# Kernel optimization log

Hardware: AMD Instinct MI355X
Metric: run time of the kernel (lower is better)

## Reference

```python
import jax, jax.numpy as jnp
import numpy as np

EMB = 512
HEADS = 8
HEAD_DIM = EMB // HEADS


def setup_inputs() -> dict:
    key = jax.random.key(0)
    ks = jax.random.split(key, 8)
    S, B = 2048, 2
    q = jax.random.normal(ks[0], (S, B, EMB), dtype=jnp.float32)
    k = jax.random.normal(ks[1], (S, B, EMB), dtype=jnp.float32)
    v = jax.random.normal(ks[2], (S, B, EMB), dtype=jnp.float32)
    sc = 1.0 / np.sqrt(HEAD_DIM)
    Wq = jax.random.normal(ks[3], (HEAD_DIM, HEAD_DIM), dtype=jnp.float32) * sc
    Wk = jax.random.normal(ks[4], (HEAD_DIM, HEAD_DIM), dtype=jnp.float32) * sc
    Wv = jax.random.normal(ks[5], (HEAD_DIM, HEAD_DIM), dtype=jnp.float32) * sc
    Wfc = jax.random.normal(ks[6], (EMB, EMB), dtype=jnp.float32) * (1.0 / np.sqrt(EMB))
    bfc = jax.random.normal(ks[7], (EMB,), dtype=jnp.float32) * 0.01
    return {"q": q, "k": k, "v": v, "Wq": Wq, "Wk": Wk, "Wv": Wv, "Wfc": Wfc, "bfc": bfc}


def reference(q, k, v, Wq, Wk, Wv, Wfc, bfc):
    query_len, batch, emb = q.shape
    key_len = k.shape[0]
    value_len = v.shape[0]
    # Faithful to the original: plain reshape (NOT transpose) from [S,B,E] -> [B,H,S,D]
    qh = q.reshape(batch, HEADS, query_len, HEAD_DIM)
    kh = k.reshape(batch, HEADS, key_len, HEAD_DIM)
    vh = v.reshape(batch, HEADS, value_len, HEAD_DIM)
    # torch Linear(head_dim, head_dim, bias=False): y = x @ W.T
    Q = qh @ Wq.T
    K = kh @ Wk.T
    V = vh @ Wv.T
    QK = jnp.einsum('bhqd,bhkd->bhqk', Q, K)  # [B,H,S,S] score matrix (memory-bound)
    filt = jax.nn.softmax(QK / np.sqrt(HEAD_DIM).astype(np.float32), axis=3)
    att = jnp.einsum('bhqk,bhkd->bhqd', filt, V)
    att = att.reshape(query_len, batch, emb)
    return att @ Wfc.T + bfc
```

## Files before the change

### kernel.cpp

```cpp
#include <hip/hip_runtime.h>
#include <hip/hip_bf16.h>


typedef __attribute__((ext_vector_type(8))) __bf16 bf16x8;
typedef __attribute__((ext_vector_type(4))) float f32x4;
typedef __attribute__((ext_vector_type(16))) float f32x16;
typedef __attribute__((ext_vector_type(4))) unsigned short u16x4;
typedef __attribute__((ext_vector_type(4))) unsigned int u32x4;
typedef __attribute__((ext_vector_type(2))) int i32x2;
typedef unsigned short u16;
typedef unsigned int u32;

static __device__ __forceinline__ u16 f2bf(float x) {
    u32 u = __float_as_uint(x);
    u += 0x7fff + ((u >> 16) & 1);
    return (u16)(u >> 16);
}
static __device__ __forceinline__ float bf2f(u16 h) {
    return __uint_as_float(((u32)h) << 16);
}
static __device__ __forceinline__ u32 pk2(float lo, float hi) {
    __hip_bfloat162 h2 = __float22bfloat162_rn(make_float2(lo, hi));
    u32 r; __builtin_memcpy(&r, &h2, 4); return r;
}
static __device__ __forceinline__ u32 cvtpk(float lo, float hi) {
    u32 r;
    asm("v_cvt_pk_bf16_f32 %0, %1, %2" : "=v"(r) : "v"(lo), "v"(hi));
    return r;
}
static __device__ __forceinline__ void halfswap(u32 &x, u32 &y) {
#if __has_builtin(__builtin_amdgcn_permlane32_swap)
    i32x2 r = __builtin_amdgcn_permlane32_swap((int)x, (int)y, false, false);
    x = (u32)r[0]; y = (u32)r[1];
#else
    int h = (threadIdx.x >> 5) & 1;
    u32 px = (u32)__shfl_xor((int)x, 32);
    u32 py = (u32)__shfl_xor((int)y, 32);
    u32 nx = h ? py : x;
    u32 ny = h ? y : px;
    x = nx; y = ny;
#endif
}
static __device__ __forceinline__ bf16x8 mk8(u32 w0, u32 w1, u32 w2, u32 w3) {
    u32x4 u = {w0, w1, w2, w3};
    bf16x8 r; __builtin_memcpy(&r, &u, 16); return r;
}

__global__ __launch_bounds__(256) void proj_kernel(
    const float* __restrict__ q, const float* __restrict__ k, const float* __restrict__ v,
    const float* __restrict__ Wq, const float* __restrict__ Wk, const float* __restrict__ Wv,
    const float* __restrict__ Wfc,
    u16* __restrict__ Qf, u16* __restrict__ Kf, u16* __restrict__ Vf,
    u16* __restrict__ Wb, float* __restrict__ KnSq)
{
    const int mode = blockIdx.z;
    const int t = threadIdx.x;

    if (mode == 3) {
        int i = (blockIdx.x * 256 + t) * 4;
        float4 val = *(const float4*)(Wfc + i);
        uint2 b = { pk2(val.x, val.y), pk2(val.z, val.w) };
        *(uint2*)(Wb + i) = b;
        return;
    }

    const float* A = (mode == 0) ? q : (mode == 1) ? k : v;
    const float* W = (mode == 0) ? Wq : (mode == 1) ? Wk : Wv;
    const float osc = (mode == 0) ? 0.18033688011112042f : 1.0f;

    __shared__ alignas(16) u16 Ash[128 * 88];
    __shared__ alignas(16) u16 Wsh[64 * 88];
    __shared__ float red[2];

    const int m0 = blockIdx.x * 128;
    const int w = t >> 6, l = t & 63;
    const int r16 = l & 15, q4 = l >> 4;

    {
        const float4* A4 = (const float4*)(A + (size_t)m0 * 64);
        const int c4 = t & 15;
        #pragma unroll
        for (int i = 0; i < 8; ++i) {
            int row = (t >> 4) + i * 16;
            float4 val = A4[row * 16 + c4];
            uint2 bb = { pk2(val.x, val.y), pk2(val.z, val.w) };
            *(uint2*)(Ash + row * 88 + c4 * 4) = bb;
        }
        const float4* W4 = (const float4*)W;
        #pragma unroll
        for (int i = 0; i < 4; ++i) {
            int row = (t >> 4) + i * 16;
            float4 val = W4[row * 16 + c4];
            uint2 bb = { pk2(val.x, val.y), pk2(val.z, val.w) };
            *(uint2*)(Wsh + row * 88 + c4 * 4) = bb;
        }
    }
    __syncthreads();

    bf16x8 af[2][2], wf[4][2];
    #pragma unroll
    for (int mc = 0; mc < 2; ++mc)
        #pragma unroll
        for (int kk = 0; kk < 2; ++kk)
            af[mc][kk] = *(const bf16x8*)(Ash + (w * 32 + mc * 16 + r16) * 88 + kk * 32 + q4 * 8);
    #pragma unroll
    for (int nc = 0; nc < 4; ++nc)
        #pragma unroll
        for (int kk = 0; kk < 2; ++kk)
            wf[nc][kk] = *(const bf16x8*)(Wsh + (nc * 16 + r16) * 88 + kk * 32 + q4 * 8);

    f32x4 acc[2][4];
    const f32x4 zero = {0.f, 0.f, 0.f, 0.f};
    #pragma unroll
    for (int mc = 0; mc < 2; ++mc)
        #pragma unroll
        for (int nc = 0; nc < 4; ++nc) {
            acc[mc][nc] = __builtin_amdgcn_mfma_f32_16x16x32_bf16(af[mc][0], wf[nc][0], zero, 0, 0, 0);
            acc[mc][nc] = __builtin_amdgcn_mfma_f32_16x16x32_bf16(af[mc][1], wf[nc][1], acc[mc][nc], 0, 0, 0);
        }

    __syncthreads();

    const int g = m0 >> 11, t0 = (m0 & 2047) >> 6;

    if (mode < 2) {
        #pragma unroll
        for (int mc = 0; mc < 2; ++mc)
            #pragma unroll
            for (int nc = 0; nc < 4; ++nc)
                #pragma unroll
                for (int r = 0; r < 4; ++r)
                    Ash[(w * 32 + mc * 16 + q4 * 4 + r) * 72 + nc * 16 + r16] = f2bf(acc[mc][nc][r] * osc);
        __syncthreads();
        u16* Out = (mode == 0) ? Qf : Kf;
        #pragma unroll
        for (int i = 0; i < 4; ++i) {
            int idx = i * 256 + t;
            int ll = idx & 63;
            int r = idx >> 6;
            int tl = r >> 3, c2 = (r >> 2) & 1, s = r & 3;
            int row = tl * 64 + c2 * 32 + (ll & 31);
            int col = s * 16 + (ll >> 5) * 8;
            u32x4 d = *(const u32x4*)(Ash + row * 72 + col);
            *(u32x4*)(Out + ((size_t)(((g * 32 + t0 + tl) * 2 + c2) * 4 + s) * 64 + ll) * 8) = d;
        }
        if (mode == 1) {
            float ss = 0.f;
            if (t < 128) {
                #pragma unroll
                for (int c = 0; c < 8; ++c) {
                    u32x4 d = *(const u32x4*)(Ash + t * 72 + c * 8);
                    #pragma unroll
                    for (int j = 0; j < 4; ++j) {
                        float lo = bf2f((u16)(d[j] & 0xffff));
                        float hi = bf2f((u16)(d[j] >> 16));
                        ss += lo * lo + hi * hi;
                    }
                }
            }
            #pragma unroll
            for (int d = 1; d < 64; d <<= 1)
                ss = fmaxf(ss, __shfl_xor(ss, d));
            if (t < 128 && (t & 63) == 0) red[t >> 6] = ss;
            __syncthreads();
            if (t == 0) KnSq[blockIdx.x] = fmaxf(red[0], red[1]);
        }
    } else {
        #pragma unroll
        for (int mc = 0; mc < 2; ++mc)
            #pragma unroll
            for (int nc = 0; nc < 4; ++nc)
                #pragma unroll
                for (int r = 0; r < 4; ++r)
                    Ash[(nc * 16 + r16) * 136 + w * 32 + mc * 16 + q4 * 4 + r] = f2bf(acc[mc][nc][r]);
        __syncthreads();
        #pragma unroll
        for (int i = 0; i < 4; ++i) {
            int idx = i * 256 + t;
            int ll = idx & 63;
            int r = idx >> 6;
            int tl = r >> 3, kh = (r >> 2) & 1, dc = (r >> 1) & 1, s2 = r & 1;
            int d = dc * 32 + (ll & 31);
            int keycol = tl * 64 + kh * 32 + s2 * 16 + (ll >> 5) * 8;
            u32x4 val = *(const u32x4*)(Ash + d * 136 + keycol);
            *(u32x4*)(Vf + ((size_t)((((g * 32 + t0 + tl) * 2 + kh) * 2 + dc) * 2 + s2) * 64 + ll) * 8) = val;
        }
    }
}

__global__ __launch_bounds__(512, 4) void flash_kernel(
    const u16* __restrict__ Qf, const u16* __restrict__ Kf,
    const u16* __restrict__ Vf, const float* __restrict__ KnSq,
    u16* __restrict__ Att)
{
    const int bi = blockIdx.x;
    const int g = bi & 15;
    const int qt = bi >> 4;
    const int t = threadIdx.x, w = t >> 6, l = t & 63;
    const int q5 = l & 31, h = l >> 5;
    const int qs = w >> 2;
    const int kq = w & 3;
    const int kh2 = kq & 1, th = kq >> 1;

    __shared__ alignas(16) unsigned char smem[61440];

    const u16* qbase = Qf + ((size_t)(((g * 32 + qt) * 2 + qs) * 4)) * 512 + l * 8;
    const u16* kbase = Kf + ((size_t)(((g * 32 + th * 16) * 2 + kh2) * 4)) * 512 + l * 8;
    const u16* vbase = Vf + ((size_t)((((g * 32 + th * 16) * 2 + kh2) * 2) * 2)) * 512 + l * 8;

    bf16x8 qb[4];
    #pragma unroll
    for (int s = 0; s < 4; ++s) qb[s] = *(const bf16x8*)(qbase + s * 512);

    float m;
    {
        float kss = KnSq[g * 16 + (l & 15)];
        kss = fmaxf(kss, __shfl_xor(kss, 1));
        kss = fmaxf(kss, __shfl_xor(kss, 2));
        kss = fmaxf(kss, __shfl_xor(kss, 4));
        kss = fmaxf(kss, __shfl_xor(kss, 8));
        float ss = 0.f;
        #pragma unroll
        for (int s = 0; s < 4; ++s)
            #pragma unroll
            for (int j = 0; j < 8; ++j) {
                float x = (float)qb[s][j];
                ss += x * x;
            }
        ss += __shfl_xor(ss, 32);
        m = sqrtf(ss * kss) * 1.0002f;
    }

    f32x16 mC, o0, o1;
    #pragma unroll
    for (int r = 0; r < 16; ++r) { mC[r] = -m; o0[r] = 0.f; o1[r] = 0.f; }
    float ls = 0.f;

    for (int it = 0; it < 16; ++it) {
        const size_t ofs = (size_t)it * 4096;
        bf16x8 ka0 = *(const bf16x8*)(kbase + ofs);
        bf16x8 ka1 = *(const bf16x8*)(kbase + ofs + 512);
        bf16x8 ka2 = *(const bf16x8*)(kbase + ofs + 1024);
        bf16x8 ka3 = *(const bf16x8*)(kbase + ofs + 1536);
        bf16x8 va0 = *(const bf16x8*)(vbase + ofs);
        bf16x8 va1 = *(const bf16x8*)(vbase + ofs + 512);
        bf16x8 va2 = *(const bf16x8*)(vbase + ofs + 1024);
        bf16x8 va3 = *(const bf16x8*)(vbase + ofs + 1536);

        f32x16 s;
        s = __builtin_amdgcn_mfma_f32_32x32x16_bf16(ka0, qb[0], mC, 0, 0, 0);
        s = __builtin_amdgcn_mfma_f32_32x32x16_bf16(ka1, qb[1], s, 0, 0, 0);
        s = __builtin_amdgcn_mfma_f32_32x32x16_bf16(ka2, qb[2], s, 0, 0, 0);
        s = __builtin_amdgcn_mfma_f32_32x32x16_bf16(ka3, qb[3], s, 0, 0, 0);

        #pragma unroll
        for (int r = 0; r < 16; ++r) { s[r] = exp2f(s[r]); ls += s[r]; }

        u32 a0 = cvtpk(s[0],  s[1]),  a1 = cvtpk(s[2],  s[3]);
        u32 b0 = cvtpk(s[4],  s[5]),  b1 = cvtpk(s[6],  s[7]);
        u32 c0 = cvtpk(s[8],  s[9]),  c1 = cvtpk(s[10], s[11]);
        u32 d0 = cvtpk(s[12], s[13]), d1 = cvtpk(s[14], s[15]);
        halfswap(a0, b0); halfswap(a1, b1);
        halfswap(c0, d0); halfswap(c1, d1);
        bf16x8 pa0 = mk8(a0, a1, b0, b1);
        bf16x8 pa1 = mk8(c0, c1, d0, d1);

        o0 = __builtin_amdgcn_mfma_f32_32x32x16_bf16(va0, pa0, o0, 0, 0, 0);
        o0 = __builtin_amdgcn_mfma_f32_32x32x16_bf16(va1, pa1, o0, 0, 0, 0);
        o1 = __builtin_amdgcn_mfma_f32_32x32x16_bf16(va2, pa0, o1, 0, 0, 0);
        o1 = __builtin_amdgcn_mfma_f32_32x32x16_bf16(va3, pa1, o1, 0, 0, 0);
    }

    float psq = ls + __shfl_xor(ls, 32);

    float* const Fsh = (float*)smem;
    u16*  const Osh = (u16*)(smem + 52224);

    __syncthreads();
    if (kq != 0) {
        float* fp = Fsh + ((qs * 3) + (kq - 1)) * (64 * 34) + l * 34;
        #pragma unroll
        for (int r = 0; r < 16; ++r) { fp[r] = o0[r]; fp[16 + r] = o1[r]; }
        fp[32] = psq;
    }
    __syncthreads();
    if (kq == 0) {
        float ltot = psq;
        #pragma unroll
        for (int b = 0; b < 3; ++b) {
            const float* fp = Fsh + (qs * 3 + b) * (64 * 34) + l * 34;
            ltot += fp[32];
            #pragma unroll
            for (int r = 0; r < 16; ++r) { o0[r] += fp[r]; o1[r] += fp[16 + r]; }
        }
        float inv = 1.0f / ltot;
        const int qloc = qs * 32 + q5;
        #pragma unroll
        for (int u = 0; u < 4; ++u) {
            uint2 w0 = { pk2(o0[4*u+0] * inv, o0[4*u+1] * inv),
                         pk2(o0[4*u+2] * inv, o0[4*u+3] * inv) };
            *(uint2*)(Osh + qloc * 72 + 8 * u + 4 * h) = w0;
            uint2 w1 = { pk2(o1[4*u+0] * inv, o1[4*u+1] * inv),
                         pk2(o1[4*u+2] * inv, o1[4*u+3] * inv) };
            *(uint2*)(Osh + qloc * 72 + 32 + 8 * u + 4 * h) = w1;
        }
    }
    __syncthreads();
    {
        int row = t >> 3, cb = (t & 7) * 8;
        u16* dst = Att + ((size_t)(g * 2048 + qt * 64 + row)) * 64 + cb;
        *(u32x4*)(dst) = *(const u32x4*)(Osh + row * 72 + cb);
    }
}

__global__ __launch_bounds__(256) void fc_kernel(
    const u16* __restrict__ Att, const u16* __restrict__ Wb,
    const float* __restrict__ bfc, float* __restrict__ out)
{
    __shared__ alignas(16) u16 Ash[2][2][64 * 64];
    __shared__ alignas(16) u16 Wsh[2][2][64 * 64];

    const int t = threadIdx.x, w = t >> 6, l = t & 63;
    const int r16 = l & 15, q4 = l >> 4;
    const int r7 = r16 & 7;
    const int m0 = blockIdx.x * 64, n0 = blockIdx.y * 64;

    const int rr = t >> 3, ck = t & 7;
    const int sw0 = (ck ^ (rr & 7)) * 8;
    const int fr0 = (q4 ^ r7) * 8;
    const int fr1 = ((q4 + 4) ^ r7) * 8;

    {
        #pragma unroll
        for (int hh = 0; hh < 2; ++hh)
            #pragma unroll
            for (int s = 0; s < 2; ++s) {
                int row = hh * 32 + rr;
                int kof = s * 64 + ck * 8;
                *(u32x4*)(&Ash[0][s][row * 64 + sw0]) = *(const u32x4*)(Att + (size_t)(m0 + row) * 512 + kof);
                *(u32x4*)(&Wsh[0][s][row * 64 + sw0]) = *(const u32x4*)(Wb + (size_t)(n0 + row) * 512 + kof);
            }
    }
    __syncthreads();

    f32x4 acc[4];
    const f32x4 zero = {0.f, 0.f, 0.f, 0.f};
    #pragma unroll
    for (int nc = 0; nc < 4; ++nc) acc[nc] = zero;

    for (int c = 0; c < 4; ++c) {
        const int cur = c & 1;
        const bool hasn = (c < 3);

        u32x4 an[4], wn[4];
        if (hasn) {
            #pragma unroll
            for (int hh = 0; hh < 2; ++hh)
                #pragma unroll
                for (int s = 0; s < 2; ++s) {
                    int row = hh * 32 + rr;
                    int kof = (c + 1) * 128 + s * 64 + ck * 8;
                    an[hh * 2 + s] = *(const u32x4*)(Att + (size_t)(m0 + row) * 512 + kof);
                    wn[hh * 2 + s] = *(const u32x4*)(Wb + (size_t)(n0 + row) * 512 + kof);
                }
        }

        #pragma unroll
        for (int s = 0; s < 2; ++s) {
            bf16x8 af0 = *(const bf16x8*)(&Ash[cur][s][(w * 16 + r16) * 64 + fr0]);
            bf16x8 af1 = *(const bf16x8*)(&Ash[cur][s][(w * 16 + r16) * 64 + fr1]);
            #pragma unroll
            for (int nc = 0; nc < 4; ++nc) {
                bf16x8 wf0 = *(const bf16x8*)(&Wsh[cur][s][(nc * 16 + r16) * 64 + fr0]);
                bf16x8 wf1 = *(const bf16x8*)(&Wsh[cur][s][(nc * 16 + r16) * 64 + fr1]);
                acc[nc] = __builtin_amdgcn_mfma_f32_16x16x32_bf16(af0, wf0, acc[nc], 0, 0, 0);
                acc[nc] = __builtin_amdgcn_mfma_f32_16x16x32_bf16(af1, wf1, acc[nc], 0, 0, 0);
            }
        }

        if (hasn) {
            const int nxt = cur ^ 1;
            #pragma unroll
            for (int hh = 0; hh < 2; ++hh)
                #pragma unroll
                for (int s = 0; s < 2; ++s) {
                    int row = hh * 32 + rr;
                    *(u32x4*)(&Ash[nxt][s][row * 64 + sw0]) = an[hh * 2 + s];
                    *(u32x4*)(&Wsh[nxt][s][row * 64 + sw0]) = wn[hh * 2 + s];
                }
        }
        __syncthreads();
    }

    #pragma unroll
    for (int nc = 0; nc < 4; ++nc) {
        float bb = bfc[n0 + nc * 16 + r16];
        #pragma unroll
        for (int r = 0; r < 4; ++r) {
            int row = m0 + w * 16 + q4 * 4 + r;
            out[(size_t)row * 512 + n0 + nc * 16 + r16] = acc[nc][r] + bb;
        }
    }
}

extern "C" void kernel_launch(void* const* d_in, const int* in_sizes, int n_in,
                              void* d_out, int out_size, void* d_ws, size_t ws_size,
                              hipStream_t stream) {
    (void)in_sizes; (void)n_in; (void)out_size; (void)ws_size;
    const float* q   = (const float*)d_in[0];
    const float* k   = (const float*)d_in[1];
    const float* v   = (const float*)d_in[2];
    const float* Wq  = (const float*)d_in[3];
    const float* Wk  = (const float*)d_in[4];
    const float* Wv  = (const float*)d_in[5];
    const float* Wfc = (const float*)d_in[6];
    const float* bfc = (const float*)d_in[7];
    float* out = (float*)d_out;

    u16* Qf = (u16*)d_ws;
    u16* Kf = Qf + 2097152;
    u16* Vf = Kf + 2097152;
    u16* At = Vf + 2097152;
    u16* Wb = At + 2097152;
    float* KnSq = (float*)((char*)d_ws + 17301504);

    proj_kernel<<<dim3(256, 1, 4), 256, 0, stream>>>(q, k, v, Wq, Wk, Wv, Wfc,
                                                     Qf, Kf, Vf, Wb, KnSq);
    flash_kernel<<<dim3(512), 512, 0, stream>>>(Qf, Kf, Vf, KnSq, At);
    fc_kernel<<<dim3(64, 8), 256, 0, stream>>>(At, Wb, bfc, out);
}
```

Baseline: 119.5 us.

## Split flash blocks across 8 key chunks with tree reduction, doubling grid

Each flash block now handles 32 query rows instead of 64. Its 8 warps each process a separate eighth of the keys (8 iterations instead of 16), and the grid doubles to 1024 blocks. Partial outputs and softmax sums are combined through a three-level shared-memory tree reduction, and shared memory per block shrinks. The aim is more parallelism and shorter per-warp serial loops, at the cost of more reduction barriers and Q fragments loaded twice as often.

```diff
diff --git a/kernel.cpp b/kernel.cpp
--- a/kernel.cpp
+++ b/kernel.cpp
@@ -195,18 +195,18 @@
 {
     const int bi = blockIdx.x;
     const int g = bi & 15;
-    const int qt = bi >> 4;
+    const int qs = (bi >> 4) & 1;
+    const int qt = bi >> 5;
     const int t = threadIdx.x, w = t >> 6, l = t & 63;
     const int q5 = l & 31, h = l >> 5;
-    const int qs = w >> 2;
-    const int kq = w & 3;
-    const int kh2 = kq & 1, th = kq >> 1;
-
-    __shared__ alignas(16) unsigned char smem[61440];
+    const int kq = w;
+    const int kh2 = kq & 1, to = kq >> 1;
+
+    __shared__ alignas(16) unsigned char smem[39424];
 
     const u16* qbase = Qf + ((size_t)(((g * 32 + qt) * 2 + qs) * 4)) * 512 + l * 8;
-    const u16* kbase = Kf + ((size_t)(((g * 32 + th * 16) * 2 + kh2) * 4)) * 512 + l * 8;
-    const u16* vbase = Vf + ((size_t)((((g * 32 + th * 16) * 2 + kh2) * 2) * 2)) * 512 + l * 8;
+    const u16* kbase = Kf + ((size_t)(((g * 32 + to * 8) * 2 + kh2) * 4)) * 512 + l * 8;
+    const u16* vbase = Vf + ((size_t)((((g * 32 + to * 8) * 2 + kh2) * 2) * 2)) * 512 + l * 8;
 
     bf16x8 qb[4];
     #pragma unroll
@@ -236,7 +236,7 @@
     for (int r = 0; r < 16; ++r) { mC[r] = -m; o0[r] = 0.f; o1[r] = 0.f; }
     float ls = 0.f;
 
-    for (int it = 0; it < 16; ++it) {
+    for (int it = 0; it < 8; ++it) {
         const size_t ofs = (size_t)it * 4096;
         bf16x8 ka0 = *(const bf16x8*)(kbase + ofs);
         bf16x8 ka1 = *(const bf16x8*)(kbase + ofs + 512);
@@ -274,41 +274,63 @@
     float psq = ls + __shfl_xor(ls, 32);
 
     float* const Fsh = (float*)smem;
-    u16*  const Osh = (u16*)(smem + 52224);
-
-    __syncthreads();
-    if (kq != 0) {
-        float* fp = Fsh + ((qs * 3) + (kq - 1)) * (64 * 34) + l * 34;
+    u16*  const Osh = (u16*)(smem + 34816);
+
+    if (kq >= 4) {
+        float* fp = Fsh + (kq - 4) * (64 * 34) + l * 34;
         #pragma unroll
         for (int r = 0; r < 16; ++r) { fp[r] = o0[r]; fp[16 + r] = o1[r]; }
         fp[32] = psq;
     }
     __syncthreads();
+    if (kq < 4) {
+        const float* fp = Fsh + kq * (64 * 34) + l * 34;
+        psq += fp[32];
+        #pragma unroll
+        for (int r = 0; r < 16; ++r) { o0[r] += fp[r]; o1[r] += fp[16 + r]; }
+    }
+    __syncthreads();
+    if (kq == 2 || kq == 3) {
+        float* fp = Fsh + (kq - 2) * (64 * 34) + l * 34;
+        #pragma unroll
+        for (int r = 0; r < 16; ++r) { fp[r] = o0[r]; fp[16 + r] = o1[r]; }
+        fp[32] = psq;
+    }
+    __syncthreads();
+    if (kq < 2) {
+        const float* fp = Fsh + kq * (64 * 34) + l * 34;
+        psq += fp[32];
+        #pragma unroll
+        for (int r = 0; r < 16; ++r) { o0[r] += fp[r]; o1[r] += fp[16 + r]; }
+    }
+    __syncthreads();
+    if (kq == 1) {
+        float* fp = Fsh + l * 34;
+        #pragma unroll
+        for (int r = 0; r < 16; ++r) { fp[r] = o0[r]; fp[16 + r] = o1[r]; }
+        fp[32] = psq;
+    }
+    __syncthreads();
     if (kq == 0) {
-        float ltot = psq;
-        #pragma unroll
-        for (int b = 0; b < 3; ++b) {
-            const float* fp = Fsh + (qs * 3 + b) * (64 * 34) + l * 34;
-            ltot += fp[32];
-            #pragma unroll
-            for (int r = 0; r < 16; ++r) { o0[r] += fp[r]; o1[r] += fp[16 + r]; }
-        }
+        const float* fp = Fsh + l * 34;
+        float ltot = psq + fp[32];
+        #pragma unroll
+        for (int r = 0; r < 16; ++r) { o0[r] += fp[r]; o1[r] += fp[16 + r]; }
         float inv = 1.0f / ltot;
-        const int qloc = qs * 32 + q5;
         #pragma unroll
         for (int u = 0; u < 4; ++u) {
             uint2 w0 = { pk2(o0[4*u+0] * inv, o0[4*u+1] * inv),
                          pk2(o0[4*u+2] * inv, o0[4*u+3] * inv) };
-            *(uint2*)(Osh + qloc * 72 + 8 * u + 4 * h) = w0;
+            *(uint2*)(Osh + q5 * 72 + 8 * u + 4 * h) = w0;
             uint2 w1 = { pk2(o1[4*u+0] * inv, o1[4*u+1] * inv),
                          pk2(o1[4*u+2] * inv, o1[4*u+3] * inv) };
-            *(uint2*)(Osh + qloc * 72 + 32 + 8 * u + 4 * h) = w1;
-        }
-    }
-    __syncthreads();
-    {
+            *(uint2*)(Osh + q5 * 72 + 32 + 8 * u + 4 * h) = w1;
+        }
+    }
+    __syncthreads();
+    if (t < 256) {
         int row = t >> 3, cb = (t & 7) * 8;
-        u16* dst = Att + ((size_t)(g * 2048 + qt * 64 + row)) * 64 + cb;
+        u16* dst = Att + ((size_t)(g * 2048 + qt * 64 + qs * 32 + row)) * 64 + cb;
         *(u32x4*)(dst) = *(const u32x4*)(Osh + row * 72 + cb);
     }
 }
@@ -426,6 +448,6 @@
 
     proj_kernel<<<dim3(256, 1, 4), 256, 0, stream>>>(q, k, v, Wq, Wk, Wv, Wfc,
                                                      Qf, Kf, Vf, Wb, KnSq);
-    flash_kernel<<<dim3(512), 512, 0, stream>>>(Qf, Kf, Vf, KnSq, At);
+    flash_kernel<<<dim3(1024), 512, 0, stream>>>(Qf, Kf, Vf, KnSq, At);
     fc_kernel<<<dim3(64, 8), 256, 0, stream>>>(At, Wb, bfc, out);
 }
```

Measured after the change: 120.1 us. About the same (+0.5%).
